# Optimization experiments

Measured on AMD Instinct MI355X. Metric: run time of the kernel, lower is better.

The kernel has to match this reference:

```python
import jax, jax.numpy as jnp
import numpy as np

EMBED_DIM = 768
NUM_HEADS = 12
FF_DIM = 3072
HEAD_DIM = EMBED_DIM // NUM_HEADS
LN_EPS = 1e-5


def setup_inputs() -> dict:
    key = jax.random.key(0)
    ks = jax.random.split(key, 10)
    C, F = EMBED_DIM, FF_DIM
    s = lambda d: 1.0 / np.sqrt(d)
    return {
        "x": jax.random.normal(ks[0], (2, 2048, C), dtype=jnp.float32),
        "w_qkv": jax.random.normal(ks[1], (C, 3 * C), dtype=jnp.float32) * s(C),
        "w_out": jax.random.normal(ks[2], (C, C), dtype=jnp.float32) * s(C),
        "ln1_g": jnp.ones((C,), jnp.float32),
        "ln1_b": jnp.zeros((C,), jnp.float32),
        "ln2_g": jnp.ones((C,), jnp.float32),
        "ln2_b": jnp.zeros((C,), jnp.float32),
        "w1": jax.random.normal(ks[3], (C, F), dtype=jnp.float32) * s(C),
        "b1": jnp.zeros((F,), jnp.float32),
        "w2": jax.random.normal(ks[4], (F, C), dtype=jnp.float32) * s(F),
        "b2": jnp.zeros((C,), jnp.float32),
    }


def _layernorm(x, g, b):
    mu = jnp.mean(x, axis=-1, keepdims=True)
    var = jnp.var(x, axis=-1, keepdims=True)
    return (x - mu) * jax.lax.rsqrt(var + LN_EPS) * g + b


def _attention(x, w_qkv, w_out):
    B, T, C = x.shape
    qkv = x @ w_qkv                               # [B,T,3C]
    q, k, v = jnp.split(qkv, 3, axis=2)
    def heads(t):  # [B,T,C] -> [B,H,T,Dh]
        return t.reshape(B, T, NUM_HEADS, HEAD_DIM).transpose(0, 2, 1, 3)
    q, k, v = heads(q), heads(k), heads(v)
    att = jnp.einsum("bhqd,bhkd->bhqk", q, k) / np.sqrt(HEAD_DIM)
    mask = jnp.tril(jnp.ones((T, T), bool))
    att = jnp.where(mask, att, -jnp.inf)
    att = jax.nn.softmax(att, axis=-1)
    out = jnp.einsum("bhqk,bhkd->bhqd", att, v)   # [B,H,T,Dh]
    out = out.transpose(0, 2, 1, 3).reshape(B, T, C)
    return out @ w_out


def reference(x, w_qkv, w_out, ln1_g, ln1_b, ln2_g, ln2_b, w1, b1, w2, b2):
    x = x + _attention(_layernorm(x, ln1_g, ln1_b), w_qkv, w_out)
    h = _layernorm(x, ln2_g, ln2_b)
    h = jax.nn.gelu(h @ w1 + b1, approximate=False) @ w2 + b2
    return x + h
```

## Files before the change

### kernel.cpp

```cpp
#include <hip/hip_runtime.h>
#include <hip/hip_bf16.h>
#include <math.h>

typedef __attribute__((ext_vector_type(8))) short short8;
typedef __attribute__((ext_vector_type(4))) float f32x4;
typedef __attribute__((address_space(1))) const void CG;
typedef __attribute__((address_space(3))) void LS;

#define LOAD_LDS16(src, dst) __builtin_amdgcn_global_load_lds((CG*)(src), (LS*)(dst), 16, 0, 0)

__device__ __forceinline__ short f2bf(float f) {
  union { float f; unsigned u; } v; v.f = f;
  unsigned r = v.u + 0x7fffu + ((v.u >> 16) & 1u);
  return (short)(r >> 16);
}

__global__ __launch_bounds__(256) void transp_all(const float* __restrict__ w_qkv,
                                                  const float* __restrict__ w_out,
                                                  const float* __restrict__ w1,
                                                  const float* __restrict__ w2,
                                                  short* __restrict__ wqkvT,
                                                  short* __restrict__ woutT,
                                                  short* __restrict__ w1T,
                                                  short* __restrict__ w2T) {
  __shared__ short t[32][33];
  int bid = blockIdx.x;
  const float* W; short* Wt; int K, N, nx, id;
  if (bid < 1728)      { W = w_qkv; Wt = wqkvT; K = 768;  N = 2304; nx = 72; id = bid; }
  else if (bid < 2304) { W = w_out; Wt = woutT; K = 768;  N = 768;  nx = 24; id = bid - 1728; }
  else if (bid < 4608) { W = w1;    Wt = w1T;   K = 768;  N = 3072; nx = 96; id = bid - 2304; }
  else                 { W = w2;    Wt = w2T;   K = 3072; N = 768;  nx = 24; id = bid - 4608; }
  int n0 = (id % nx) << 5, k0 = (id / nx) << 5;
  int tid = threadIdx.x;
#pragma unroll
  for (int p = 0; p < 4; ++p) {
    int e = tid + (p << 8);
    int r = e >> 5, c = e & 31;
    t[r][c] = f2bf(W[(size_t)(k0 + r) * N + n0 + c]);
  }
  __syncthreads();
#pragma unroll
  for (int p = 0; p < 4; ++p) {
    int e = tid + (p << 8);
    int r = e >> 5, c = e & 31;
    Wt[(size_t)(n0 + r) * K + k0 + c] = t[c][r];
  }
}

__global__ __launch_bounds__(256) void ln_kernel(const float* __restrict__ x,
                                                 const float* __restrict__ g,
                                                 const float* __restrict__ b,
                                                 short* __restrict__ out) {
  int row = blockIdx.x;
  const float* xr = x + (size_t)row * 768;
  int tid = threadIdx.x;
  float v0 = xr[tid], v1 = xr[tid + 256], v2 = xr[tid + 512];
  float s = v0 + v1 + v2;
  float ss = v0 * v0 + v1 * v1 + v2 * v2;
#pragma unroll
  for (int m = 1; m < 64; m <<= 1) { s += __shfl_xor(s, m); ss += __shfl_xor(ss, m); }
  __shared__ float red[8];
  int w = tid >> 6;
  if ((tid & 63) == 0) { red[w] = s; red[w + 4] = ss; }
  __syncthreads();
  s = red[0] + red[1] + red[2] + red[3];
  ss = red[4] + red[5] + red[6] + red[7];
  float mean = s * (1.0f / 768.0f);
  float var = ss * (1.0f / 768.0f) - mean * mean;
  float rs = rsqrtf(var + 1e-5f);
  short* outr = out + (size_t)row * 768;
  outr[tid]       = f2bf((v0 - mean) * rs * g[tid]       + b[tid]);
  outr[tid + 256] = f2bf((v1 - mean) * rs * g[tid + 256] + b[tid + 256]);
  outr[tid + 512] = f2bf((v2 - mean) * rs * g[tid + 512] + b[tid + 512]);
}

template <int EPI>
__global__ __launch_bounds__(256, 3) void gemm_bt(
    const short* __restrict__ A, const short* __restrict__ Bt,
    int M, int N, int K,
    short* __restrict__ outQ, short* __restrict__ outK, short* __restrict__ outVt,
    float* __restrict__ outF, short* __restrict__ outB,
    const float* __restrict__ bias, const float* __restrict__ resid) {
  __shared__ short lA[3][128 * 32];
  __shared__ short lB[3][128 * 32];
  int tid = threadIdx.x;
  int lane = tid & 63, w = tid >> 6;
  int li = lane & 15, g = lane >> 4;

  int nx = gridDim.x, ny = gridDim.y;
  int nwg = nx * ny;
  int fid = (int)blockIdx.y * nx + (int)blockIdx.x;
  int nid = (fid & 7) * (nwg >> 3) + (fid >> 3);
  const int GM = 8;
  int npg = GM * nx;
  int grp = nid / npg;
  int fm = grp * GM;
  int gs = min(GM, ny - fm);
  int lid = nid - grp * npg;
  int bm = (fm + lid % gs) << 7;
  int bn = (lid / gs) << 7;

  int wrow = (w >> 1) << 6, wcol = (w & 1) << 6;
  size_t lda = (EPI == 4) ? 3072 : (size_t)K;
  int koff = (EPI == 4) ? (int)blockIdx.z * 1536 : 0;

  const short* as[2];
  const short* bs[2];
#pragma unroll
  for (int p = 0; p < 2; ++p) {
    int v = tid + (p << 8);
    int row = v >> 2;
    int lc = (v & 3) ^ ((row ^ (row >> 2)) & 3);
    as[p] = A + (size_t)(bm + row) * lda + koff + lc * 8;
    bs[p] = Bt + (size_t)(bn + row) * lda + koff + lc * 8;
  }
  int sg = (g ^ ((li ^ (li >> 2)) & 3)) << 3;

  f32x4 zero = {0.f, 0.f, 0.f, 0.f};
  f32x4 acc[4][4];
#pragma unroll
  for (int i = 0; i < 4; ++i)
#pragma unroll
    for (int j = 0; j < 4; ++j) acc[i][j] = zero;

#define GSTAGE(buf, ki)                                                 \
  do {                                                                  \
    int kk = (ki) << 5;                                                 \
    LOAD_LDS16(as[0] + kk, (char*)lA[buf] + (w << 10));                 \
    LOAD_LDS16(as[1] + kk, (char*)lA[buf] + 4096 + (w << 10));          \
    LOAD_LDS16(bs[0] + kk, (char*)lB[buf] + (w << 10));                 \
    LOAD_LDS16(bs[1] + kk, (char*)lB[buf] + 4096 + (w << 10));          \
  } while (0)

  auto compute = [&](int bufidx) {
    const short* lAc = lA[bufidx];
    const short* lBc = lB[bufidx];
    short8 af[4], bf[4];
#pragma unroll
    for (int rt = 0; rt < 4; ++rt)
      af[rt] = *(const short8*)&lAc[(wrow + rt * 16 + li) * 32 + sg];
#pragma unroll
    for (int ct = 0; ct < 4; ++ct)
      bf[ct] = *(const short8*)&lBc[(wcol + ct * 16 + li) * 32 + sg];
#pragma unroll
    for (int rt = 0; rt < 4; ++rt)
#pragma unroll
      for (int ct = 0; ct < 4; ++ct)
        acc[rt][ct] = __builtin_amdgcn_mfma_f32_16x16x32_bf16(af[rt], bf[ct], acc[rt][ct], 0, 0, 0);
  };

  int nk = K >> 5;
  GSTAGE(0, 0);
  GSTAGE(1, 1);
  int cur = 0, n1 = 1, n2 = 2;
  for (int ki = 0; ki < nk - 1; ++ki) {
    asm volatile("s_waitcnt vmcnt(4)" ::: "memory");
    __builtin_amdgcn_s_barrier();
    __builtin_amdgcn_sched_barrier(0);
    if (ki + 2 < nk) GSTAGE(n2, ki + 2);
    compute(cur);
    int t = cur; cur = n1; n1 = n2; n2 = t;
  }
  asm volatile("s_waitcnt vmcnt(0)" ::: "memory");
  __builtin_amdgcn_s_barrier();
  __builtin_amdgcn_sched_barrier(0);
  compute(cur);
#undef GSTAGE

#pragma unroll
  for (int rt = 0; rt < 4; ++rt) {
    int mbase = bm + wrow + rt * 16 + g * 4;
#pragma unroll
    for (int ct = 0; ct < 4; ++ct) {
      int n = bn + wcol + ct * 16 + li;
      f32x4 c = acc[rt][ct];
      if (EPI == 0) {
        if (n < 768) {
          int h = n >> 6, d = n & 63;
#pragma unroll
          for (int i = 0; i < 4; ++i) {
            int tok = mbase + i;
            int bb = tok >> 11, t = tok & 2047;
            outQ[((size_t)((bb * 12 + h) * 2048 + t) << 6) + d] = f2bf(c[i]);
          }
        } else if (n < 1536) {
          int nn = n - 768;
          int h = nn >> 6, d = nn & 63;
#pragma unroll
          for (int i = 0; i < 4; ++i) {
            int tok = mbase + i;
            int bb = tok >> 11, t = tok & 2047;
            outK[((size_t)((bb * 12 + h) * 2048 + t) << 6) + d] = f2bf(c[i]);
          }
        } else {
          int nn = n - 1536;
          int h = nn >> 6, d = nn & 63;
          int bb = mbase >> 11, t = mbase & 2047;
          ushort4 pk;
          pk.x = (unsigned short)f2bf(c[0]);
          pk.y = (unsigned short)f2bf(c[1]);
          pk.z = (unsigned short)f2bf(c[2]);
          pk.w = (unsigned short)f2bf(c[3]);
          *(ushort4*)((unsigned short*)outVt + (((size_t)((bb * 12 + h) * 64 + d)) << 11) + t) = pk;
        }
      } else if (EPI == 1) {
#pragma unroll
        for (int i = 0; i < 4; ++i) {
          int m = mbase + i;
          outF[(size_t)m * N + n] = c[i] + resid[(size_t)m * N + n];
        }
      } else if (EPI == 2) {
        float bv = bias[n];
#pragma unroll
        for (int i = 0; i < 4; ++i) {
          int m = mbase + i;
          float xx = c[i] + bv;
          float gel = 0.5f * xx * (1.0f + erff(xx * 0.70710678118654752f));
          outB[(size_t)m * N + n] = f2bf(gel);
        }
      } else if (EPI == 3) {
        float bv = bias[n];
#pragma unroll
        for (int i = 0; i < 4; ++i) {
          int m = mbase + i;
          outF[(size_t)m * N + n] = c[i] + bv + resid[(size_t)m * N + n];
        }
      } else {
        bool last = (blockIdx.z == 1);
        float bv = last ? bias[n] : 0.f;
#pragma unroll
        for (int i = 0; i < 4; ++i) {
          int m = mbase + i;
          float add = c[i] + bv + (last ? resid[(size_t)m * N + n] : 0.f);
          atomicAdd(&outF[(size_t)m * N + n], add);
        }
      }
    }
  }
}

__global__ __launch_bounds__(256, 3) void attn_kernel(const short* __restrict__ Q,
                                                      const short* __restrict__ Kk,
                                                      const short* __restrict__ Vt,
                                                      unsigned short* __restrict__ o_part,
                                                      float* __restrict__ ml_part) {
  __shared__ short lK[2][64 * 64];
  __shared__ short lV[2][64 * 64];
  __shared__ short lP[4][32 * 64];
  int tid = threadIdx.x;
  int lane = tid & 63, w = tid >> 6;
  int li = lane & 15, g = lane >> 4;
  int bh = blockIdx.y;
  int cid = 39 - (int)blockIdx.x;
  int qt = 0, cum = 0;
  while (true) { int n = (qt >> 2) + 1; if (cid < cum + n) break; cum += n; ++qt; }
  int c = cid - cum;
  int nch = (qt >> 2) + 1;
  int nt = (qt + 1) << 1;
  int bq = nt / nch, rem = nt % nch;
  int t0 = c * bq + (c < rem ? c : rem);
  int t1 = t0 + bq + (c < rem ? 1 : 0);

  int qbase = (qt << 7) + (w << 5);
  const short* Qb = Q + ((size_t)bh << 17);
  const short* Kb = Kk + ((size_t)bh << 17);
  const short* Vb = Vt + ((size_t)bh << 17);

  short8 qf[2][2];
#pragma unroll
  for (int rt = 0; rt < 2; ++rt)
#pragma unroll
    for (int kc = 0; kc < 2; ++kc)
      qf[rt][kc] = *(const short8*)&Qb[(size_t)(qbase + rt * 16 + li) * 64 + kc * 32 + g * 8];

  int r0 = tid >> 3, s0 = (tid & 7) ^ (r0 & 7);
  int r1 = r0 + 32,  s1 = (tid & 7) ^ (r1 & 7);
  const short* kS0 = Kb + r0 * 64 + s0 * 8;
  const short* kS1 = Kb + r1 * 64 + s1 * 8;
  const short* vS0 = Vb + (size_t)r0 * 2048 + s0 * 8;
  const short* vS1 = Vb + (size_t)r1 * 2048 + s1 * 8;

#define STAGE(buf, kt)                                                        \
  do {                                                                        \
    LOAD_LDS16(kS0 + (size_t)(kt) * 4096, (char*)lK[buf] + (w << 10));        \
    LOAD_LDS16(kS1 + (size_t)(kt) * 4096, (char*)lK[buf] + 4096 + (w << 10)); \
    LOAD_LDS16(vS0 + (size_t)(kt) * 64,   (char*)lV[buf] + (w << 10));        \
    LOAD_LDS16(vS1 + (size_t)(kt) * 64,   (char*)lV[buf] + 4096 + (w << 10)); \
  } while (0)

  const short8 kOnes = {0x3F80, 0x3F80, 0x3F80, 0x3F80, 0x3F80, 0x3F80, 0x3F80, 0x3F80};
  f32x4 zero = {0.f, 0.f, 0.f, 0.f};
  f32x4 o[2][4];
  f32x4 lrow[2];
  float mrow[2] = {-1e30f, -1e30f};
#pragma unroll
  for (int rt = 0; rt < 2; ++rt) {
    lrow[rt] = zero;
#pragma unroll
    for (int ct = 0; ct < 4; ++ct) o[rt][ct] = zero;
  }

  int diagKt = qbase >> 6;
  const float SCALE = 0.18033688011112042f;
  int sw = li & 7;
  unsigned short* Pw = (unsigned short*)lP[w];

  STAGE(0, t0);

  for (int kt = t0; kt < t1; ++kt) {
    int cur = (kt - t0) & 1;
    __syncthreads();
    if (kt + 1 < t1) STAGE(cur ^ 1, kt + 1);

    if (kt <= diagKt) {
      const short* Kc = lK[cur];
      const short* Vc = lV[cur];

      f32x4 s[2][4];
#pragma unroll
      for (int rt = 0; rt < 2; ++rt)
#pragma unroll
        for (int ct = 0; ct < 4; ++ct) s[rt][ct] = zero;
#pragma unroll
      for (int kc = 0; kc < 2; ++kc)
#pragma unroll
        for (int ct = 0; ct < 4; ++ct) {
          short8 kf = *(const short8*)&Kc[(ct * 16 + li) * 64 + ((((kc << 2) | g) ^ sw) << 3)];
#pragma unroll
          for (int rt = 0; rt < 2; ++rt)
            s[rt][ct] = __builtin_amdgcn_mfma_f32_16x16x32_bf16(qf[rt][kc], kf, s[rt][ct], 0, 0, 0);
        }

      if (kt == diagKt) {
        int kb0 = kt << 6;
#pragma unroll
        for (int rt = 0; rt < 2; ++rt) {
          int qrow0 = qbase + rt * 16 + g * 4;
#pragma unroll
          for (int ct = 0; ct < 4; ++ct) {
            int kcol = kb0 + ct * 16 + li;
#pragma unroll
            for (int i = 0; i < 4; ++i)
              if (kcol > qrow0 + i) s[rt][ct][i] = -1e30f;
          }
        }
      }

#pragma unroll
      for (int rt = 0; rt < 2; ++rt) {
        float tm = s[rt][0][0];
#pragma unroll
        for (int ct = 0; ct < 4; ++ct)
#pragma unroll
          for (int i = 0; i < 4; ++i) tm = fmaxf(tm, s[rt][ct][i]);
#pragma unroll
        for (int m2 = 1; m2 < 64; m2 <<= 1) tm = fmaxf(tm, __shfl_xor(tm, m2));
        if (tm > mrow[rt] + 8.0f) {
          float corr = exp2f((mrow[rt] - tm) * SCALE);
          mrow[rt] = tm;
#pragma unroll
          for (int i = 0; i < 4; ++i) lrow[rt][i] *= corr;
#pragma unroll
          for (int ct = 0; ct < 4; ++ct)
#pragma unroll
            for (int i = 0; i < 4; ++i) o[rt][ct][i] *= corr;
        }
#pragma unroll
        for (int ct = 0; ct < 4; ++ct)
#pragma unroll
          for (int i = 0; i < 4; ++i) {
            float p = exp2f((s[rt][ct][i] - mrow[rt]) * SCALE);
            int row = rt * 16 + (g << 2) + i;
            int col = (ct << 4) + li;
            int ch = (col >> 3) ^ (row & 7);
            Pw[(row << 6) + (ch << 3) + (col & 7)] = (unsigned short)f2bf(p);
          }
      }

      f32x4 psum[2];
      psum[0] = zero; psum[1] = zero;
#pragma unroll
      for (int kc = 0; kc < 2; ++kc) {
        short8 vf[4];
#pragma unroll
        for (int ct = 0; ct < 4; ++ct)
          vf[ct] = *(const short8*)&Vc[(ct * 16 + li) * 64 + ((((kc << 2) | g) ^ sw) << 3)];
#pragma unroll
        for (int rt = 0; rt < 2; ++rt) {
          short8 pf = *(const short8*)&lP[w][(rt * 16 + li) * 64 + ((((kc << 2) | g) ^ sw) << 3)];
#pragma unroll
          for (int ct = 0; ct < 4; ++ct)
            o[rt][ct] = __builtin_amdgcn_mfma_f32_16x16x32_bf16(pf, vf[ct], o[rt][ct], 0, 0, 0);
          psum[rt] = __builtin_amdgcn_mfma_f32_16x16x32_bf16(pf, kOnes, psum[rt], 0, 0, 0);
        }
      }
#pragma unroll
      for (int rt = 0; rt < 2; ++rt)
#pragma unroll
        for (int i = 0; i < 4; ++i) lrow[rt][i] += psum[rt][i];
    }
  }
#undef STAGE

  int pid = bh * 40 + cid;
#pragma unroll
  for (int rt = 0; rt < 2; ++rt)
#pragma unroll
    for (int ct = 0; ct < 4; ++ct) {
      int col = (ct << 4) + li;
      int row0 = (w << 5) + (rt << 4) + (g << 2);
      ushort4 pk;
      pk.x = (unsigned short)f2bf(o[rt][ct][0]);
      pk.y = (unsigned short)f2bf(o[rt][ct][1]);
      pk.z = (unsigned short)f2bf(o[rt][ct][2]);
      pk.w = (unsigned short)f2bf(o[rt][ct][3]);
      *(ushort4*)&o_part[((size_t)pid * 64 + col) * 128 + row0] = pk;
    }
  if (li == 0) {
    float2* mlp = (float2*)ml_part;
#pragma unroll
    for (int rt = 0; rt < 2; ++rt)
#pragma unroll
      for (int i = 0; i < 4; ++i) {
        int row = (w << 5) + (rt << 4) + (g << 2) + i;
        mlp[(size_t)pid * 128 + row] = make_float2(mrow[rt], lrow[rt][i]);
      }
  }
}

__global__ __launch_bounds__(256) void attn_combine(const unsigned short* __restrict__ o_part,
                                                    const float* __restrict__ ml_part,
                                                    short* __restrict__ O) {
  __shared__ float wgt[4][128];
  int qt = blockIdx.x, bh = blockIdx.y;
  int a = qt >> 2, bb = qt & 3;
  int c0 = 2 * a * (a - 1) + a * bb + qt;
  int nch = a + 1;
  int pid0 = bh * 40 + c0;
  int tid = threadIdx.x;
  const float SCALE = 0.18033688011112042f;
  const float2* mlp = (const float2*)ml_part;

  if (tid < 128) {
    int row = tid;
    float mv[4] = {-1e30f, -1e30f, -1e30f, -1e30f};
    float lv[4] = {0.f, 0.f, 0.f, 0.f};
#pragma unroll
    for (int c = 0; c < 4; ++c)
      if (c < nch) {
        float2 ml = mlp[(size_t)(pid0 + c) * 128 + row];
        mv[c] = ml.x; lv[c] = ml.y;
      }
    float M = fmaxf(fmaxf(mv[0], mv[1]), fmaxf(mv[2], mv[3]));
    float u[4];
    float L = 0.f;
#pragma unroll
    for (int c = 0; c < 4; ++c) {
      u[c] = (c < nch) ? exp2f((mv[c] - M) * SCALE) : 0.f;
      L += lv[c] * u[c];
    }
    float inv = 1.0f / L;
#pragma unroll
    for (int c = 0; c < 4; ++c) wgt[c][row] = u[c] * inv;
  }
  __syncthreads();

  int col = tid & 63, rg = tid >> 6;
  int b = bh / 12, h = bh % 12;
  size_t obase[4];
#pragma unroll
  for (int c = 0; c < 4; ++c) obase[c] = ((size_t)(pid0 + c) * 64 + col) * 128;
  for (int r = 0; r < 32; ++r) {
    int row = (rg << 5) + r;
    float acc = 0.f;
#pragma unroll
    for (int c = 0; c < 4; ++c)
      if (c < nch) {
        union { unsigned u; float f; } cv;
        cv.u = ((unsigned)o_part[obase[c] + row]) << 16;
        acc += cv.f * wgt[c][row];
      }
    int t = (qt << 7) + row;
    O[((size_t)(b * 2048 + t)) * 768 + h * 64 + col] = f2bf(acc);
  }
}

extern "C" void kernel_launch(void* const* d_in, const int* in_sizes, int n_in,
                              void* d_out, int out_size, void* d_ws, size_t ws_size,
                              hipStream_t stream) {
  const float* x     = (const float*)d_in[0];
  const float* w_qkv = (const float*)d_in[1];
  const float* w_out = (const float*)d_in[2];
  const float* ln1g  = (const float*)d_in[3];
  const float* ln1b  = (const float*)d_in[4];
  const float* ln2g  = (const float*)d_in[5];
  const float* ln2b  = (const float*)d_in[6];
  const float* w1    = (const float*)d_in[7];
  const float* b1    = (const float*)d_in[8];
  const float* w2    = (const float*)d_in[9];
  const float* b2    = (const float*)d_in[10];
  float* out = (float*)d_out;
  char* ws = (char*)d_ws;

  short* wqkvT = (short*)(ws + 0);
  short* woutT = (short*)(ws + 3538944);
  short* w1T   = (short*)(ws + 4718592);
  short* w2T   = (short*)(ws + 9437184);
  short* qb    = (short*)(ws + 14155776);
  short* kb    = (short*)(ws + 20447232);
  short* vtb   = (short*)(ws + 26738688);
  short* attnb = (short*)(ws + 33030144);
  short* ab    = qb;
  short* xnb   = (short*)(ws + 39321600);
  float* x2b   = (float*)(ws + 45613056);
  unsigned short* o_part = (unsigned short*)(ws + 39321600);
  float* ml_part = (float*)(ws + 55050240);

  transp_all<<<dim3(6912), 256, 0, stream>>>(w_qkv, w_out, w1, w2, wqkvT, woutT, w1T, w2T);

  ln_kernel<<<dim3(4096), 256, 0, stream>>>(x, ln1g, ln1b, xnb);

  gemm_bt<0><<<dim3(18, 32), 256, 0, stream>>>(xnb, wqkvT, 4096, 2304, 768,
                                               qb, kb, vtb, nullptr, nullptr, nullptr, nullptr);

  attn_kernel<<<dim3(40, 24), 256, 0, stream>>>(qb, kb, vtb, o_part, ml_part);
  attn_combine<<<dim3(16, 24), 256, 0, stream>>>(o_part, ml_part, attnb);

  gemm_bt<1><<<dim3(6, 32), 256, 0, stream>>>(attnb, woutT, 4096, 768, 768,
                                              nullptr, nullptr, nullptr, x2b, nullptr, nullptr, x);

  ln_kernel<<<dim3(4096), 256, 0, stream>>>(x2b, ln2g, ln2b, xnb);

  gemm_bt<2><<<dim3(24, 32), 256, 0, stream>>>(xnb, w1T, 4096, 3072, 768,
                                               nullptr, nullptr, nullptr, nullptr, ab, b1, nullptr);

  hipMemsetAsync(out, 0, (size_t)4096 * 768 * 4, stream);
  gemm_bt<4><<<dim3(6, 32, 2), 256, 0, stream>>>(ab, w2T, 4096, 768, 1536,
                                                 nullptr, nullptr, nullptr, out, nullptr, b2, x2b);
}
```

Measured before the change: 245.4 us.

## Add 256x256-tile 8-wave GEMM for QKV, FFN1 and FFN2 with split-K 4

Adds a new GEMM kernel that uses 256x256 output tiles with 512 threads, a K-step of 64, double-buffered LDS and an XOR swizzle. It replaces the 128x128 kernel for the QKV, FFN1 and FFN2 GEMMs, and FFN2 now uses 4-way split-K instead of 2-way. The goal is more data reuse per LDS load and fewer global loads per FLOP. The cost is fewer workgroups, which can leave the 256 CUs underfilled (144 and 192 blocks), and a simpler two-stage pipeline with full __syncthreads. The out-projection GEMM keeps the old kernel with a trimmed signature.

Measured after the change: 284.4 us. 1.16x slower.

```diff
diff --git a/kernel.cpp b/kernel.cpp
--- a/kernel.cpp
+++ b/kernel.cpp
@@ -75,17 +75,18 @@
 }
 
 template <int EPI>
-__global__ __launch_bounds__(256, 3) void gemm_bt(
+__global__ __launch_bounds__(512, 2) void gemm256(
     const short* __restrict__ A, const short* __restrict__ Bt,
     int M, int N, int K,
     short* __restrict__ outQ, short* __restrict__ outK, short* __restrict__ outVt,
     float* __restrict__ outF, short* __restrict__ outB,
     const float* __restrict__ bias, const float* __restrict__ resid) {
-  __shared__ short lA[3][128 * 32];
-  __shared__ short lB[3][128 * 32];
+  __shared__ short lA[2][256 * 64];
+  __shared__ short lB[2][256 * 64];
   int tid = threadIdx.x;
   int lane = tid & 63, w = tid >> 6;
   int li = lane & 15, g = lane >> 4;
+  int wr = w >> 2, wc = w & 3;
 
   int nx = gridDim.x, ny = gridDim.y;
   int nwg = nx * ny;
@@ -97,82 +98,75 @@
   int fm = grp * GM;
   int gs = min(GM, ny - fm);
   int lid = nid - grp * npg;
-  int bm = (fm + lid % gs) << 7;
-  int bn = (lid / gs) << 7;
-
-  int wrow = (w >> 1) << 6, wcol = (w & 1) << 6;
+  int bm = (fm + lid % gs) << 8;
+  int bn = (lid / gs) << 8;
+
   size_t lda = (EPI == 4) ? 3072 : (size_t)K;
-  int koff = (EPI == 4) ? (int)blockIdx.z * 1536 : 0;
-
-  const short* as[2];
-  const short* bs[2];
-#pragma unroll
-  for (int p = 0; p < 2; ++p) {
-    int v = tid + (p << 8);
-    int row = v >> 2;
-    int lc = (v & 3) ^ ((row ^ (row >> 2)) & 3);
-    as[p] = A + (size_t)(bm + row) * lda + koff + lc * 8;
-    bs[p] = Bt + (size_t)(bn + row) * lda + koff + lc * 8;
-  }
-  int sg = (g ^ ((li ^ (li >> 2)) & 3)) << 3;
+  int koff = (EPI == 4) ? (int)blockIdx.z * 768 : 0;
+
+  int r8 = lane >> 3, cph = lane & 7;
+  int csrc = cph ^ r8;
+  const short* asA[4];
+  const short* bsB[4];
+#pragma unroll
+  for (int p = 0; p < 4; ++p) {
+    int row = p * 64 + w * 8 + r8;
+    asA[p] = A + (size_t)(bm + row) * lda + koff + csrc * 8;
+    bsB[p] = Bt + (size_t)(bn + row) * lda + koff + csrc * 8;
+  }
+
+#define STG(buf, ki)                                                      \
+  do {                                                                    \
+    int kk = (ki) << 6;                                                   \
+    LOAD_LDS16(asA[0] + kk, (char*)lA[buf] + (w << 10));                  \
+    LOAD_LDS16(asA[1] + kk, (char*)lA[buf] + 8192 + (w << 10));           \
+    LOAD_LDS16(asA[2] + kk, (char*)lA[buf] + 16384 + (w << 10));          \
+    LOAD_LDS16(asA[3] + kk, (char*)lA[buf] + 24576 + (w << 10));          \
+    LOAD_LDS16(bsB[0] + kk, (char*)lB[buf] + (w << 10));                  \
+    LOAD_LDS16(bsB[1] + kk, (char*)lB[buf] + 8192 + (w << 10));           \
+    LOAD_LDS16(bsB[2] + kk, (char*)lB[buf] + 16384 + (w << 10));          \
+    LOAD_LDS16(bsB[3] + kk, (char*)lB[buf] + 24576 + (w << 10));          \
+  } while (0)
 
   f32x4 zero = {0.f, 0.f, 0.f, 0.f};
-  f32x4 acc[4][4];
-#pragma unroll
-  for (int i = 0; i < 4; ++i)
+  f32x4 acc[8][4];
+#pragma unroll
+  for (int i = 0; i < 8; ++i)
 #pragma unroll
     for (int j = 0; j < 4; ++j) acc[i][j] = zero;
 
-#define GSTAGE(buf, ki)                                                 \
-  do {                                                                  \
-    int kk = (ki) << 5;                                                 \
-    LOAD_LDS16(as[0] + kk, (char*)lA[buf] + (w << 10));                 \
-    LOAD_LDS16(as[1] + kk, (char*)lA[buf] + 4096 + (w << 10));          \
-    LOAD_LDS16(bs[0] + kk, (char*)lB[buf] + (w << 10));                 \
-    LOAD_LDS16(bs[1] + kk, (char*)lB[buf] + 4096 + (w << 10));          \
-  } while (0)
-
-  auto compute = [&](int bufidx) {
-    const short* lAc = lA[bufidx];
-    const short* lBc = lB[bufidx];
-    short8 af[4], bf[4];
-#pragma unroll
-    for (int rt = 0; rt < 4; ++rt)
-      af[rt] = *(const short8*)&lAc[(wrow + rt * 16 + li) * 32 + sg];
-#pragma unroll
-    for (int ct = 0; ct < 4; ++ct)
-      bf[ct] = *(const short8*)&lBc[(wcol + ct * 16 + li) * 32 + sg];
-#pragma unroll
-    for (int rt = 0; rt < 4; ++rt)
+  int nk = K >> 6;
+  STG(0, 0);
+  for (int ki = 0; ki < nk; ++ki) {
+    int cur = ki & 1;
+    __syncthreads();
+    if (ki + 1 < nk) STG(cur ^ 1, ki + 1);
+    const short* Ac = lA[cur];
+    const short* Bc = lB[cur];
+#pragma unroll
+    for (int kc = 0; kc < 2; ++kc) {
+      int ch = (((kc << 2) | g) ^ (li & 7)) << 3;
+      short8 bf[4];
 #pragma unroll
       for (int ct = 0; ct < 4; ++ct)
-        acc[rt][ct] = __builtin_amdgcn_mfma_f32_16x16x32_bf16(af[rt], bf[ct], acc[rt][ct], 0, 0, 0);
-  };
-
-  int nk = K >> 5;
-  GSTAGE(0, 0);
-  GSTAGE(1, 1);
-  int cur = 0, n1 = 1, n2 = 2;
-  for (int ki = 0; ki < nk - 1; ++ki) {
-    asm volatile("s_waitcnt vmcnt(4)" ::: "memory");
-    __builtin_amdgcn_s_barrier();
-    __builtin_amdgcn_sched_barrier(0);
-    if (ki + 2 < nk) GSTAGE(n2, ki + 2);
-    compute(cur);
-    int t = cur; cur = n1; n1 = n2; n2 = t;
-  }
-  asm volatile("s_waitcnt vmcnt(0)" ::: "memory");
-  __builtin_amdgcn_s_barrier();
-  __builtin_amdgcn_sched_barrier(0);
-  compute(cur);
-#undef GSTAGE
-
-#pragma unroll
-  for (int rt = 0; rt < 4; ++rt) {
-    int mbase = bm + wrow + rt * 16 + g * 4;
+        bf[ct] = *(const short8*)&Bc[(wc * 64 + ct * 16 + li) * 64 + ch];
+#pragma unroll
+      for (int rt = 0; rt < 8; ++rt) {
+        short8 af = *(const short8*)&Ac[(wr * 128 + rt * 16 + li) * 64 + ch];
+#pragma unroll
+        for (int ct = 0; ct < 4; ++ct)
+          acc[rt][ct] = __builtin_amdgcn_mfma_f32_16x16x32_bf16(af, bf[ct], acc[rt][ct], 0, 0, 0);
+      }
+    }
+  }
+#undef STG
+
+#pragma unroll
+  for (int rt = 0; rt < 8; ++rt) {
+    int mbase = bm + wr * 128 + rt * 16 + g * 4;
 #pragma unroll
     for (int ct = 0; ct < 4; ++ct) {
-      int n = bn + wcol + ct * 16 + li;
+      int n = bn + wc * 64 + ct * 16 + li;
       f32x4 c = acc[rt][ct];
       if (EPI == 0) {
         if (n < 768) {
@@ -203,12 +197,6 @@
           pk.w = (unsigned short)f2bf(c[3]);
           *(ushort4*)((unsigned short*)outVt + (((size_t)((bb * 12 + h) * 64 + d)) << 11) + t) = pk;
         }
-      } else if (EPI == 1) {
-#pragma unroll
-        for (int i = 0; i < 4; ++i) {
-          int m = mbase + i;
-          outF[(size_t)m * N + n] = c[i] + resid[(size_t)m * N + n];
-        }
       } else if (EPI == 2) {
         float bv = bias[n];
 #pragma unroll
@@ -218,15 +206,8 @@
           float gel = 0.5f * xx * (1.0f + erff(xx * 0.70710678118654752f));
           outB[(size_t)m * N + n] = f2bf(gel);
         }
-      } else if (EPI == 3) {
-        float bv = bias[n];
-#pragma unroll
-        for (int i = 0; i < 4; ++i) {
-          int m = mbase + i;
-          outF[(size_t)m * N + n] = c[i] + bv + resid[(size_t)m * N + n];
-        }
       } else {
-        bool last = (blockIdx.z == 1);
+        bool last = (blockIdx.z == 3);
         float bv = last ? bias[n] : 0.f;
 #pragma unroll
         for (int i = 0; i < 4; ++i) {
@@ -234,6 +215,111 @@
           float add = c[i] + bv + (last ? resid[(size_t)m * N + n] : 0.f);
           atomicAdd(&outF[(size_t)m * N + n], add);
         }
+      }
+    }
+  }
+}
+
+template <int EPI>
+__global__ __launch_bounds__(256, 3) void gemm_bt(
+    const short* __restrict__ A, const short* __restrict__ Bt,
+    int M, int N, int K,
+    float* __restrict__ outF, const float* __restrict__ resid) {
+  __shared__ short lA[3][128 * 32];
+  __shared__ short lB[3][128 * 32];
+  int tid = threadIdx.x;
+  int lane = tid & 63, w = tid >> 6;
+  int li = lane & 15, g = lane >> 4;
+
+  int nx = gridDim.x, ny = gridDim.y;
+  int nwg = nx * ny;
+  int fid = (int)blockIdx.y * nx + (int)blockIdx.x;
+  int nid = (fid & 7) * (nwg >> 3) + (fid >> 3);
+  const int GM = 8;
+  int npg = GM * nx;
+  int grp = nid / npg;
+  int fm = grp * GM;
+  int gs = min(GM, ny - fm);
+  int lid = nid - grp * npg;
+  int bm = (fm + lid % gs) << 7;
+  int bn = (lid / gs) << 7;
+
+  int wrow = (w >> 1) << 6, wcol = (w & 1) << 6;
+
+  const short* as[2];
+  const short* bs[2];
+#pragma unroll
+  for (int p = 0; p < 2; ++p) {
+    int v = tid + (p << 8);
+    int row = v >> 2;
+    int lc = (v & 3) ^ ((row ^ (row >> 2)) & 3);
+    as[p] = A + (size_t)(bm + row) * K + lc * 8;
+    bs[p] = Bt + (size_t)(bn + row) * K + lc * 8;
+  }
+  int sg = (g ^ ((li ^ (li >> 2)) & 3)) << 3;
+
+  f32x4 zero = {0.f, 0.f, 0.f, 0.f};
+  f32x4 acc[4][4];
+#pragma unroll
+  for (int i = 0; i < 4; ++i)
+#pragma unroll
+    for (int j = 0; j < 4; ++j) acc[i][j] = zero;
+
+#define GSTAGE(buf, ki)                                                 \
+  do {                                                                  \
+    int kk = (ki) << 5;                                                 \
+    LOAD_LDS16(as[0] + kk, (char*)lA[buf] + (w << 10));                 \
+    LOAD_LDS16(as[1] + kk, (char*)lA[buf] + 4096 + (w << 10));          \
+    LOAD_LDS16(bs[0] + kk, (char*)lB[buf] + (w << 10));                 \
+    LOAD_LDS16(bs[1] + kk, (char*)lB[buf] + 4096 + (w << 10));          \
+  } while (0)
+
+  auto compute = [&](int bufidx) {
+    const short* lAc = lA[bufidx];
+    const short* lBc = lB[bufidx];
+    short8 af[4], bf[4];
+#pragma unroll
+    for (int rt = 0; rt < 4; ++rt)
+      af[rt] = *(const short8*)&lAc[(wrow + rt * 16 + li) * 32 + sg];
+#pragma unroll
+    for (int ct = 0; ct < 4; ++ct)
+      bf[ct] = *(const short8*)&lBc[(wcol + ct * 16 + li) * 32 + sg];
+#pragma unroll
+    for (int rt = 0; rt < 4; ++rt)
+#pragma unroll
+      for (int ct = 0; ct < 4; ++ct)
+        acc[rt][ct] = __builtin_amdgcn_mfma_f32_16x16x32_bf16(af[rt], bf[ct], acc[rt][ct], 0, 0, 0);
+  };
+
+  int nk = K >> 5;
+  GSTAGE(0, 0);
+  GSTAGE(1, 1);
+  int cur = 0, n1 = 1, n2 = 2;
+  for (int ki = 0; ki < nk - 1; ++ki) {
+    asm volatile("s_waitcnt vmcnt(4)" ::: "memory");
+    __builtin_amdgcn_s_barrier();
+    __builtin_amdgcn_sched_barrier(0);
+    if (ki + 2 < nk) GSTAGE(n2, ki + 2);
+    compute(cur);
+    int t = cur; cur = n1; n1 = n2; n2 = t;
+  }
+  asm volatile("s_waitcnt vmcnt(0)" ::: "memory");
+  __builtin_amdgcn_s_barrier();
+  __builtin_amdgcn_sched_barrier(0);
+  compute(cur);
+#undef GSTAGE
+
+#pragma unroll
+  for (int rt = 0; rt < 4; ++rt) {
+    int mbase = bm + wrow + rt * 16 + g * 4;
+#pragma unroll
+    for (int ct = 0; ct < 4; ++ct) {
+      int n = bn + wcol + ct * 16 + li;
+      f32x4 c = acc[rt][ct];
+#pragma unroll
+      for (int i = 0; i < 4; ++i) {
+        int m = mbase + i;
+        outF[(size_t)m * N + n] = c[i] + resid[(size_t)m * N + n];
       }
     }
   }
@@ -520,21 +606,20 @@
 
   ln_kernel<<<dim3(4096), 256, 0, stream>>>(x, ln1g, ln1b, xnb);
 
-  gemm_bt<0><<<dim3(18, 32), 256, 0, stream>>>(xnb, wqkvT, 4096, 2304, 768,
-                                               qb, kb, vtb, nullptr, nullptr, nullptr, nullptr);
+  gemm256<0><<<dim3(9, 16), 512, 0, stream>>>(xnb, wqkvT, 4096, 2304, 768,
+                                              qb, kb, vtb, nullptr, nullptr, nullptr, nullptr);
 
   attn_kernel<<<dim3(40, 24), 256, 0, stream>>>(qb, kb, vtb, o_part, ml_part);
   attn_combine<<<dim3(16, 24), 256, 0, stream>>>(o_part, ml_part, attnb);
 
-  gemm_bt<1><<<dim3(6, 32), 256, 0, stream>>>(attnb, woutT, 4096, 768, 768,
-                                              nullptr, nullptr, nullptr, x2b, nullptr, nullptr, x);
+  gemm_bt<1><<<dim3(6, 32), 256, 0, stream>>>(attnb, woutT, 4096, 768, 768, x2b, x);
 
   ln_kernel<<<dim3(4096), 256, 0, stream>>>(x2b, ln2g, ln2b, xnb);
 
-  gemm_bt<2><<<dim3(24, 32), 256, 0, stream>>>(xnb, w1T, 4096, 3072, 768,
+  gemm256<2><<<dim3(12, 16), 512, 0, stream>>>(xnb, w1T, 4096, 3072, 768,
                                                nullptr, nullptr, nullptr, nullptr, ab, b1, nullptr);
 
   hipMemsetAsync(out, 0, (size_t)4096 * 768 * 4, stream);
-  gemm_bt<4><<<dim3(6, 32, 2), 256, 0, stream>>>(ab, w2T, 4096, 768, 1536,
+  gemm256<4><<<dim3(3, 16, 4), 512, 0, stream>>>(ab, w2T, 4096, 768, 768,
                                                  nullptr, nullptr, nullptr, out, nullptr, b2, x2b);
 }
```
